# Optimization experiments

Hardware: AMD Instinct MI355X
Metric: run time of the kernel (lower is better)

## Reference

```python
import jax, jax.numpy as jnp
import numpy as np

N_NODES = 100000
N_EDGES = 1600000
DIM_IN = 128
DIM_OUT = 64


def _spmm(edge_row, edge_col, edge_vals, X):
    # DAD.mm(X): sparse COO [N,N] times dense [N,d]
    # gather source features, scale by edge value, scatter-add to rows
    msgs = edge_vals[:, None] * X[edge_col]          # [E, d]
    return jax.ops.segment_sum(msgs, edge_row, num_segments=N_NODES)


def setup_inputs() -> dict:
    key = jax.random.key(0)
    k1, k2, k3, k4, k5, k6 = jax.random.split(key, 6)
    X = jax.random.normal(k1, (N_NODES, DIM_IN), dtype=jnp.float32)
    W1 = jax.random.normal(k2, (DIM_IN, DIM_IN), dtype=jnp.float32) * (1.0 / np.sqrt(DIM_IN))
    W2 = jax.random.normal(k3, (DIM_OUT, DIM_IN), dtype=jnp.float32) * (1.0 / np.sqrt(DIM_IN))
    edge_vals = jax.random.uniform(k4, (N_EDGES,), dtype=jnp.float32)
    edge_row = jax.random.randint(k5, (N_EDGES,), 0, N_NODES, dtype=jnp.int32)
    edge_col = jax.random.randint(k6, (N_EDGES,), 0, N_NODES, dtype=jnp.int32)
    return {"X": X, "W1": W1, "W2": W2, "edge_vals": edge_vals,
            "edge_row": edge_row, "edge_col": edge_col}


def reference(X, W1, W2, edge_vals, edge_row, edge_col):
    # layer 1: tanh(fc1(DAD @ X)); nn.Linear(bias=False) is x @ W.T
    h = jnp.tanh(_spmm(edge_row, edge_col, edge_vals, X) @ W1.T)
    # layer 2: tanh(fc2(DAD @ h))
    out = jnp.tanh(_spmm(edge_row, edge_col, edge_vals, h) @ W2.T)
    return out
```

## Files before the change

kernel.cpp:

```cpp
#include <hip/hip_runtime.h>
#include <hip/hip_bf16.h>
#include <hip/hip_fp16.h>

#define N_NODES 100000
#define N_EDGES 1600000
#define DIM_IN 128
#define DIM_OUT 64

#define NB 391
#define NCHUNK 391
#define CHUNK 4096
#define BCAP 5120
#define EPCAP 6144

typedef unsigned int uint;
typedef unsigned short ushort;
typedef _Float16 half8 __attribute__((ext_vector_type(8)));
typedef float f32x4 __attribute__((ext_vector_type(4)));

__device__ inline ushort f2h(float f) {
    __half h = __float2half(f);
    return *reinterpret_cast<ushort*>(&h);
}


__global__ __launch_bounds__(256) void chunk_hist_kernel(const int* __restrict__ erow,
                                                         int* __restrict__ counts, int E) {
    __shared__ int hist[NB];
    const int t = threadIdx.x, c = blockIdx.x;
    for (int b = t; b < NB; b += 256) hist[b] = 0;
    __syncthreads();
    const int eb = c * CHUNK;
#pragma unroll
    for (int i = 0; i < CHUNK / 256; ++i) {
        int e = eb + i * 256 + t;
        if (e < E) atomicAdd(&hist[erow[e] >> 8], 1);
    }
    __syncthreads();
    for (int b = t; b < NB; b += 256) counts[b * NCHUNK + c] = hist[b];
}

__global__ __launch_bounds__(512) void bucket_scan_kernel(const int* __restrict__ counts,
                                                          int* __restrict__ offnb,
                                                          int* __restrict__ tot) {
    __shared__ int s[512];
    const int b = blockIdx.x, t = threadIdx.x;
    int v = (t < NCHUNK) ? counts[b * NCHUNK + t] : 0;
    s[t] = v;
    __syncthreads();
#pragma unroll
    for (int o = 1; o < 512; o <<= 1) {
        int x = s[t];
        int y = (t >= o) ? s[t - o] : 0;
        __syncthreads();
        s[t] = x + y;
        __syncthreads();
    }
    if (t < NCHUNK) offnb[b * NCHUNK + t] = s[t] - v;
    if (t == 511) tot[b] = s[511];
}

__global__ __launch_bounds__(512) void base_scan_kernel(const int* __restrict__ tot,
                                                        int* __restrict__ bbase) {
    __shared__ int s[512];
    const int t = threadIdx.x;
    int v = (t < NB) ? tot[t] : 0;
    s[t] = v;
    __syncthreads();
#pragma unroll
    for (int o = 1; o < 512; o <<= 1) {
        int x = s[t];
        int y = (t >= o) ? s[t - o] : 0;
        __syncthreads();
        s[t] = x + y;
        __syncthreads();
    }
    if (t < NB) bbase[t] = s[t] - v;
    if (t == 511) bbase[NB] = s[511];
}

__global__ __launch_bounds__(512) void coarse_scatter_kernel(const int* __restrict__ erow,
                                                             const int* __restrict__ ecol,
                                                             const float* __restrict__ eval,
                                                             const int* __restrict__ offnb,
                                                             const int* __restrict__ bbase,
                                                             uint* __restrict__ keyOut,
                                                             float* __restrict__ valOut, int E) {
    __shared__ int hist[NB];
    __shared__ int segOff[NB];
    __shared__ int localOff[NB];
    __shared__ int sc[512];
    __shared__ int idxL[CHUNK];
    __shared__ int gaddrL[CHUNK];

    const int t = threadIdx.x, c = blockIdx.x;
    for (int b = t; b < NB; b += 512) {
        hist[b] = 0;
        segOff[b] = bbase[b] + offnb[b * NCHUNK + c];
    }
    __syncthreads();
    const int eb = c * CHUNK;
    uint bq[CHUNK / 512];
#pragma unroll
    for (int i = 0; i < CHUNK / 512; ++i) {
        int e = eb + i * 512 + t;
        if (e < E) {
            int b = erow[e] >> 8;
            int q = atomicAdd(&hist[b], 1);
            bq[i] = ((uint)b << 16) | (uint)q;
        } else {
            bq[i] = 0xFFFFFFFFu;
        }
    }
    __syncthreads();
    int v = (t < NB) ? hist[t] : 0;
    sc[t] = v;
    __syncthreads();
#pragma unroll
    for (int o = 1; o < 512; o <<= 1) {
        int x = sc[t];
        int y = (t >= o) ? sc[t - o] : 0;
        __syncthreads();
        sc[t] = x + y;
        __syncthreads();
    }
    if (t < NB) localOff[t] = sc[t] - v;
    __syncthreads();
#pragma unroll
    for (int i = 0; i < CHUNK / 512; ++i) {
        if (bq[i] != 0xFFFFFFFFu) {
            int b = bq[i] >> 16;
            int q = bq[i] & 0xFFFF;
            int s = localOff[b] + q;
            idxL[s] = eb + i * 512 + t;
            gaddrL[s] = segOff[b] + q;
        }
    }
    __syncthreads();
    const int m = min(CHUNK, E - eb);
    for (int s = t; s < m; s += 512) {
        int e = idxL[s];
        int g = gaddrL[s];
        keyOut[g] = ((uint)(erow[e] & 255) << 17) | (uint)ecol[e];
        valOut[g] = eval[e];
    }
}

__global__ __launch_bounds__(256) void fine_sort_kernel(const uint* __restrict__ keyOut,
                                                        const float* __restrict__ valOut,
                                                        const int* __restrict__ bbase,
                                                        int* __restrict__ row_ptr,
                                                        int* __restrict__ row_len,
                                                        int2* __restrict__ ep) {
    __shared__ uint keyL[BCAP];
    __shared__ int hist[256];
    __shared__ int offs[256];
    const int b = blockIdx.x, t = threadIdx.x;
    const int s0 = bbase[b], s1 = bbase[b + 1];
    const int m = min(s1 - s0, BCAP);
    hist[t] = 0;
    __syncthreads();
    for (int j = t; j < m; j += 256) {
        uint k = keyOut[s0 + j];
        keyL[j] = k;
        atomicAdd(&hist[k >> 17], 1);
    }
    __syncthreads();
    const int deg = hist[t];
    const int pdeg = (deg + 7) & ~7;
    offs[t] = pdeg;
    __syncthreads();
#pragma unroll
    for (int o = 1; o < 256; o <<= 1) {
        int x = offs[t];
        int y = (t >= o) ? offs[t - o] : 0;
        __syncthreads();
        offs[t] = x + y;
        __syncthreads();
    }
    const int pexcl = offs[t] - pdeg;
    const int base = b * EPCAP;
    const int row = b * 256 + t;
    if (row < N_NODES) {
        row_ptr[row] = base + pexcl;
        row_len[row] = pdeg;
    }
    hist[t] = pexcl;
    __syncthreads();
    for (int j = t; j < m; j += 256) {
        uint k = keyL[j];
        int r8 = (int)(k >> 17);
        int pos = atomicAdd(&hist[r8], 1);
        ep[base + pos] = make_int2((int)(((uint)(r8 & 15) << 17) | (k & 0x1FFFFu)),
                                   __float_as_int(valOut[s0 + j]));
    }
    __syncthreads();
    for (int j = pexcl + deg; j < pexcl + pdeg; ++j)
        ep[base + j] = make_int2((int)((uint)(t & 15) << 17), 0);
}


__global__ __launch_bounds__(256) void cvt_weights_kernel(const float* __restrict__ W1,
                                                          const float* __restrict__ W2,
                                                          uint* __restrict__ W1h,
                                                          uint* __restrict__ W2h) {
    int i = blockIdx.x * 256 + threadIdx.x;
    const float* in;
    uint* outp;
    int j;
    if (i < 2048) { in = W1; outp = W1h; j = i; }
    else if (i < 3072) { in = W2; outp = W2h; j = i - 2048; }
    else return;
    const float4* in4 = reinterpret_cast<const float4*>(in) + (size_t)j * 2;
    float4 a = in4[0];
    float4 b = in4[1];
    uint4 o;
    o.x = (uint)f2h(a.x) | ((uint)f2h(a.y) << 16);
    o.y = (uint)f2h(a.z) | ((uint)f2h(a.w) << 16);
    o.z = (uint)f2h(b.x) | ((uint)f2h(b.y) << 16);
    o.w = (uint)f2h(b.z) | ((uint)f2h(b.w) << 16);
    reinterpret_cast<uint4*>(outp)[j] = o;
}


__global__ __launch_bounds__(256) void mfma_gemm128_kernel(const float* __restrict__ Af,
                                                           const uint* __restrict__ Wh,
                                                           uint* __restrict__ Out, int M) {
    __shared__ __align__(16) ushort sA[128 * 128];
    __shared__ __align__(16) ushort sB[128 * 128];

    const int t = threadIdx.x;
    const int l = t & 63;
    const int w = t >> 6;
    const int row0 = blockIdx.x * 128;
    const int lr = l & 15;
    const int lk = l >> 4;

#pragma unroll
    for (int i = 0; i < 16; ++i) {
        int fid = i * 256 + t;
        int row = fid >> 5, q4 = fid & 31;
        int gr = row0 + row;
        float4 v = make_float4(0.f, 0.f, 0.f, 0.f);
        if (gr < M) v = *reinterpret_cast<const float4*>(Af + (size_t)gr * 128 + q4 * 4);
        uint2 p;
        p.x = (uint)f2h(v.x) | ((uint)f2h(v.y) << 16);
        p.y = (uint)f2h(v.z) | ((uint)f2h(v.w) << 16);
        int slot = q4 >> 1;
        *reinterpret_cast<uint2*>(&sA[row * 128 + ((slot ^ (row & 7)) << 3) + (q4 & 1) * 4]) = p;
    }
#pragma unroll
    for (int i = 0; i < 8; ++i) {
        int fid = i * 256 + t;
        int row = fid >> 4, slot = fid & 15;
        uint4 v = reinterpret_cast<const uint4*>(Wh)[row * 16 + slot];
        *reinterpret_cast<uint4*>(&sB[row * 128 + ((slot ^ (row & 7)) << 3)]) = v;
    }
    __syncthreads();

    f32x4 acc[2][8];
#pragma unroll
    for (int rf = 0; rf < 2; ++rf)
#pragma unroll
        for (int cf = 0; cf < 8; ++cf) acc[rf][cf] = (f32x4){0.f, 0.f, 0.f, 0.f};

    half8 aF[2][4];
#pragma unroll
    for (int rf = 0; rf < 2; ++rf) {
        int row = w * 32 + rf * 16 + lr;
#pragma unroll
        for (int kc = 0; kc < 4; ++kc) {
            int slot = kc * 4 + lk;
            aF[rf][kc] = *reinterpret_cast<const half8*>(&sA[row * 128 + ((slot ^ (row & 7)) << 3)]);
        }
    }
#pragma unroll
    for (int cf = 0; cf < 8; ++cf) {
        int col = cf * 16 + lr;
#pragma unroll
        for (int kc = 0; kc < 4; ++kc) {
            int slot = kc * 4 + lk;
            half8 bF = *reinterpret_cast<const half8*>(&sB[col * 128 + ((slot ^ (col & 7)) << 3)]);
            acc[0][cf] = __builtin_amdgcn_mfma_f32_16x16x32_f16(aF[0][kc], bF, acc[0][cf], 0, 0, 0);
            acc[1][cf] = __builtin_amdgcn_mfma_f32_16x16x32_f16(aF[1][kc], bF, acc[1][cf], 0, 0, 0);
        }
    }
    __syncthreads();

    ushort* sOut = sA;
#pragma unroll
    for (int rf = 0; rf < 2; ++rf)
#pragma unroll
        for (int cf = 0; cf < 8; ++cf)
#pragma unroll
            for (int reg = 0; reg < 4; ++reg) {
                int row = w * 32 + rf * 16 + lk * 4 + reg;
                int col = cf * 16 + lr;
                sOut[row * 128 + col] = f2h(acc[rf][cf][reg]);
            }
    __syncthreads();
#pragma unroll
    for (int i = 0; i < 8; ++i) {
        int fid = i * 256 + t;
        int row = fid >> 4, q = fid & 15;
        int gr = row0 + row;
        if (gr < M)
            reinterpret_cast<uint4*>(Out)[(size_t)gr * 16 + q] =
                *reinterpret_cast<const uint4*>(&sOut[row * 128 + q * 8]);
    }
}


__global__ __launch_bounds__(256) void spmm1_fused_kernel(const int2* __restrict__ ep,
                                                          const int* __restrict__ row_ptr,
                                                          const int* __restrict__ row_len,
                                                          const uint* __restrict__ T,
                                                          const uint* __restrict__ W2h,
                                                          uint* __restrict__ Ph, int M) {
    __shared__ __align__(16) ushort sH[16 * 128];
    __shared__ __align__(16) ushort sP[16 * 64];

    const int t = threadIdx.x;
    const int l = t & 63;
    const int w = t >> 6;
    const int lr = l & 15;
    const int lk = l >> 4;
    const int row0 = blockIdx.x * 16;

    uint* sHu = reinterpret_cast<uint*>(sH);
#pragma unroll
    for (int rr = 0; rr < 4; ++rr) {
        const int lrow = w * 4 + rr;
        const int r = row0 + lrow;
        float a0x = 0.f, a0y = 0.f, a1x = 0.f, a1y = 0.f;
        if (r < M) {
            int beg = row_ptr[r];
            int end = beg + row_len[r];
            for (int e = beg; e < end; e += 8) {
                int2 cv[8];
                uint xu[8];
#pragma unroll
                for (int i = 0; i < 8; ++i) cv[i] = ep[e + i];
#pragma unroll
                for (int i = 0; i < 8; ++i) xu[i] = T[(size_t)(cv[i].x & 0x1FFFF) * 64 + l];
#pragma unroll
                for (int i = 0; i < 8; ++i) {
                    float v = __int_as_float(cv[i].y);
                    __half2 h2 = *reinterpret_cast<__half2*>(&xu[i]);
                    float2 f = __half22float2(h2);
                    if (i & 1) { a1x += v * f.x; a1y += v * f.y; }
                    else       { a0x += v * f.x; a0y += v * f.y; }
                }
            }
        }
        uint hv = (uint)f2h(tanhf(a0x + a1x)) | ((uint)f2h(tanhf(a0y + a1y)) << 16);
        int slot = l >> 2;
        sHu[lrow * 64 + ((slot ^ (lrow & 7)) << 2) + (l & 3)] = hv;
    }
    __syncthreads();

    f32x4 acc = (f32x4){0.f, 0.f, 0.f, 0.f};
    const int col = w * 16 + lr;
#pragma unroll
    for (int kc = 0; kc < 4; ++kc) {
        const int slot = kc * 4 + lk;
        half8 aF = *reinterpret_cast<const half8*>(&sH[lr * 128 + ((slot ^ (lr & 7)) << 3)]);
        const uint4 wv = reinterpret_cast<const uint4*>(W2h)[col * 16 + slot];
        half8 bF = *reinterpret_cast<const half8*>(&wv);
        acc = __builtin_amdgcn_mfma_f32_16x16x32_f16(aF, bF, acc, 0, 0, 0);
    }
#pragma unroll
    for (int reg = 0; reg < 4; ++reg)
        sP[(lk * 4 + reg) * 64 + col] = f2h(acc[reg]);
    __syncthreads();

    if (t < 128) {
        const int row = t >> 3, q = t & 7;
        const int gr = row0 + row;
        if (gr < M)
            reinterpret_cast<uint4*>(Ph)[(size_t)gr * 8 + q] =
                *reinterpret_cast<const uint4*>(&sP[row * 64 + q * 8]);
    }
}


__global__ __launch_bounds__(256) void spmm2_kernel(const int2* __restrict__ ep,
                                                    const int* __restrict__ row_ptr,
                                                    const int* __restrict__ row_len,
                                                    const ushort* __restrict__ Ph,
                                                    float* __restrict__ out) {
    int wave = threadIdx.x >> 6;
    int lane = threadIdx.x & 63;
    int r = blockIdx.x * 4 + wave;
    if (r >= N_NODES) return;
    int beg = row_ptr[r];
    int end = beg + row_len[r];
    float acc0 = 0.f, acc1 = 0.f;
    for (int e = beg; e < end; e += 8) {
        int2 cv[8];
        ushort xu[8];
#pragma unroll
        for (int i = 0; i < 8; ++i) cv[i] = ep[e + i];
#pragma unroll
        for (int i = 0; i < 8; ++i) xu[i] = Ph[(size_t)(cv[i].x & 0x1FFFF) * 64 + lane];
#pragma unroll
        for (int i = 0; i < 8; ++i) {
            float v = __int_as_float(cv[i].y);
            __half h = *reinterpret_cast<__half*>(&xu[i]);
            float x = __half2float(h);
            if (i & 1) acc1 += v * x;
            else       acc0 += v * x;
        }
    }
    out[(size_t)r * DIM_OUT + lane] = tanhf(acc0 + acc1);
}


extern "C" void kernel_launch(void* const* d_in, const int* in_sizes, int n_in,
                              void* d_out, int out_size, void* d_ws, size_t ws_size,
                              hipStream_t stream) {
    const float* X = (const float*)d_in[0];
    const float* W1 = (const float*)d_in[1];
    const float* W2 = (const float*)d_in[2];
    const float* evals = (const float*)d_in[3];
    const int* erow = (const int*)d_in[4];
    const int* ecol = (const int*)d_in[5];
    float* out = (float*)d_out;

    const int N = N_NODES;
    const int E = N_EDGES;

    char* ws = (char*)d_ws;
    size_t off = 0;
    auto alloc = [&](size_t bytes) {
        size_t o = off;
        off = (off + bytes + 255) & ~(size_t)255;
        return o;
    };
    size_t o_counts = alloc((size_t)NB * NCHUNK * 4);
    size_t o_offnb = alloc((size_t)NB * NCHUNK * 4);
    size_t o_tot = alloc((size_t)NB * 4);
    size_t o_bbase = alloc((size_t)(NB + 1) * 4);
    size_t o_rowptr = alloc((size_t)N * 4);
    size_t o_rowlen = alloc((size_t)N * 4);
    size_t o_ep = alloc((size_t)NB * EPCAP * 8);
    size_t o_key = alloc((size_t)E * 4);
    size_t o_val = alloc((size_t)E * 4);
    size_t o_xw1 = alloc((size_t)N * 64 * 4);
    size_t o_ph = alloc((size_t)N * 32 * 4);
    size_t o_w1h = alloc((size_t)128 * 64 * 4);
    size_t o_w2h = alloc((size_t)64 * 64 * 4);
    (void)ws_size;

    int* counts = (int*)(ws + o_counts);
    int* offnb = (int*)(ws + o_offnb);
    int* tot = (int*)(ws + o_tot);
    int* bbase = (int*)(ws + o_bbase);
    int* row_ptr = (int*)(ws + o_rowptr);
    int* row_len = (int*)(ws + o_rowlen);
    int2* ep = (int2*)(ws + o_ep);
    uint* keyOut = (uint*)(ws + o_key);
    float* valOut = (float*)(ws + o_val);
    uint* XW1h = (uint*)(ws + o_xw1);
    uint* Ph = (uint*)(ws + o_ph);
    uint* W1h = (uint*)(ws + o_w1h);
    uint* W2h = (uint*)(ws + o_w2h);

    const int gemm_grid = (N + 127) / 128;
    const int spmm2_grid = (N + 3) / 4;
    const int fused_grid = N / 16;

    cvt_weights_kernel<<<12, 256, 0, stream>>>(W1, W2, W1h, W2h);
    mfma_gemm128_kernel<<<gemm_grid, 256, 0, stream>>>(X, W1h, XW1h, N);

    chunk_hist_kernel<<<NCHUNK, 256, 0, stream>>>(erow, counts, E);
    bucket_scan_kernel<<<NB, 512, 0, stream>>>(counts, offnb, tot);
    base_scan_kernel<<<1, 512, 0, stream>>>(tot, bbase);
    coarse_scatter_kernel<<<NCHUNK, 512, 0, stream>>>(erow, ecol, evals, offnb, bbase,
                                                      keyOut, valOut, E);
    fine_sort_kernel<<<NB, 256, 0, stream>>>(keyOut, valOut, bbase, row_ptr, row_len, ep);

    spmm1_fused_kernel<<<fused_grid, 256, 0, stream>>>(ep, row_ptr, row_len, XW1h, W2h, Ph, N);
    spmm2_kernel<<<spmm2_grid, 256, 0, stream>>>(ep, row_ptr, row_len, (const ushort*)Ph, out);
}
```

Before: 204.0 us.

## Make each wave own 16 rows in fused SpMM1 to drop block barriers

```diff
diff --git a/kernel.cpp b/kernel.cpp
--- a/kernel.cpp
+++ b/kernel.cpp
@@ -317,25 +317,25 @@
                                                           const uint* __restrict__ T,
                                                           const uint* __restrict__ W2h,
                                                           uint* __restrict__ Ph, int M) {
-    __shared__ __align__(16) ushort sH[16 * 128];
-    __shared__ __align__(16) ushort sP[16 * 64];
+    __shared__ __align__(16) ushort sH[64 * 128];
+    __shared__ __align__(16) ushort sP[64 * 64];
 
     const int t = threadIdx.x;
     const int l = t & 63;
     const int w = t >> 6;
     const int lr = l & 15;
     const int lk = l >> 4;
-    const int row0 = blockIdx.x * 16;
+    const int row0 = blockIdx.x * 64;
+    const int wrow0 = w * 16;
 
     uint* sHu = reinterpret_cast<uint*>(sH);
-#pragma unroll
-    for (int rr = 0; rr < 4; ++rr) {
-        const int lrow = w * 4 + rr;
+    for (int rr = 0; rr < 16; ++rr) {
+        const int lrow = wrow0 + rr;
         const int r = row0 + lrow;
         float a0x = 0.f, a0y = 0.f, a1x = 0.f, a1y = 0.f;
         if (r < M) {
-            int beg = row_ptr[r];
-            int end = beg + row_len[r];
+            const int beg = row_ptr[r];
+            const int end = beg + row_len[r];
             for (int e = beg; e < end; e += 8) {
                 int2 cv[8];
                 uint xu[8];
@@ -353,33 +353,49 @@
                 }
             }
         }
-        uint hv = (uint)f2h(tanhf(a0x + a1x)) | ((uint)f2h(tanhf(a0y + a1y)) << 16);
-        int slot = l >> 2;
+        const uint hv = (uint)f2h(tanhf(a0x + a1x)) | ((uint)f2h(tanhf(a0y + a1y)) << 16);
+        const int slot = l >> 2;
         sHu[lrow * 64 + ((slot ^ (lrow & 7)) << 2) + (l & 3)] = hv;
     }
-    __syncthreads();
-
-    f32x4 acc = (f32x4){0.f, 0.f, 0.f, 0.f};
-    const int col = w * 16 + lr;
-#pragma unroll
-    for (int kc = 0; kc < 4; ++kc) {
-        const int slot = kc * 4 + lk;
-        half8 aF = *reinterpret_cast<const half8*>(&sH[lr * 128 + ((slot ^ (lr & 7)) << 3)]);
-        const uint4 wv = reinterpret_cast<const uint4*>(W2h)[col * 16 + slot];
-        half8 bF = *reinterpret_cast<const half8*>(&wv);
-        acc = __builtin_amdgcn_mfma_f32_16x16x32_f16(aF, bF, acc, 0, 0, 0);
-    }
-#pragma unroll
-    for (int reg = 0; reg < 4; ++reg)
-        sP[(lk * 4 + reg) * 64 + col] = f2h(acc[reg]);
-    __syncthreads();
-
-    if (t < 128) {
-        const int row = t >> 3, q = t & 7;
-        const int gr = row0 + row;
+    __threadfence_block();
+
+    half8 aF[4];
+    {
+        const int arow = wrow0 + lr;
+#pragma unroll
+        for (int kc = 0; kc < 4; ++kc) {
+            const int slot = kc * 4 + lk;
+            aF[kc] = *reinterpret_cast<const half8*>(&sH[arow * 128 + ((slot ^ (arow & 7)) << 3)]);
+        }
+    }
+    f32x4 acc[4];
+#pragma unroll
+    for (int ct = 0; ct < 4; ++ct) acc[ct] = (f32x4){0.f, 0.f, 0.f, 0.f};
+#pragma unroll
+    for (int ct = 0; ct < 4; ++ct) {
+        const int col = ct * 16 + lr;
+#pragma unroll
+        for (int kc = 0; kc < 4; ++kc) {
+            const uint4 wv = reinterpret_cast<const uint4*>(W2h)[col * 16 + kc * 4 + lk];
+            half8 bF = *reinterpret_cast<const half8*>(&wv);
+            acc[ct] = __builtin_amdgcn_mfma_f32_16x16x32_f16(aF[kc], bF, acc[ct], 0, 0, 0);
+        }
+    }
+#pragma unroll
+    for (int ct = 0; ct < 4; ++ct)
+#pragma unroll
+        for (int reg = 0; reg < 4; ++reg)
+            sP[(wrow0 + lk * 4 + reg) * 64 + ct * 16 + lr] = f2h(acc[ct][reg]);
+    __threadfence_block();
+
+#pragma unroll
+    for (int i = 0; i < 2; ++i) {
+        const int fid = i * 64 + l;
+        const int prow = fid >> 3, q = fid & 7;
+        const int gr = row0 + wrow0 + prow;
         if (gr < M)
             reinterpret_cast<uint4*>(Ph)[(size_t)gr * 8 + q] =
-                *reinterpret_cast<const uint4*>(&sP[row * 64 + q * 8]);
+                *reinterpret_cast<const uint4*>(&sP[(wrow0 + prow) * 64 + q * 8]);
     }
 }
 
@@ -468,7 +484,7 @@
 
     const int gemm_grid = (N + 127) / 128;
     const int spmm2_grid = (N + 3) / 4;
-    const int fused_grid = N / 16;
+    const int fused_grid = (N + 63) / 64;
 
     cvt_weights_kernel<<<12, 256, 0, stream>>>(W1, W2, W1h, W2h);
     mfma_gemm128_kernel<<<gemm_grid, 256, 0, stream>>>(X, W1h, XW1h, N);
```

Result: slower. 231.5 us (+13.5%).
